# Kernel optimization log

Measured on AMD Instinct MI355X. Metric: run time of the kernel, lower is better.

Reference implementation:

```python
import jax, jax.numpy as jnp
import numpy as np

NUM_HEADS = 16
HEAD_DIM = 64
LN_EPS = 1e-5


def setup_inputs() -> dict:
    key = jax.random.key(0)
    k1, k2, k3, k4 = jax.random.split(key, 4)
    B, N, D = 4, 2048, NUM_HEADS * HEAD_DIM
    q = jax.random.normal(k1, (B, N, D), dtype=jnp.float32)
    k = jax.random.normal(k2, (B, N, D), dtype=jnp.float32)
    v = jax.random.normal(k3, (B, N, D), dtype=jnp.float32)
    W_out = jax.random.normal(k4, (D, D), dtype=jnp.float32) * (1.0 / np.sqrt(D))
    g = jnp.ones((D,), dtype=jnp.float32)
    return {"q": q, "k": k, "v": v, "W_out": W_out, "g": g}


def _split_heads(x):
    b, n, _ = x.shape
    return x.reshape(b, n, NUM_HEADS, HEAD_DIM).transpose(0, 2, 1, 3)  # b h n d


def reference(q, k, v, W_out, g):
    scale = HEAD_DIM ** -0.5
    qh = _split_heads(q) * scale          # [b,h,n,d]
    kh = _split_heads(k)                  # [b,h,m,d]
    vh = _split_heads(v)                  # [b,h,m,d]
    sim = jnp.einsum('bhnd,bhmd->bhnm', qh, kh)
    attn = jax.nn.softmax(sim.astype(jnp.float32), axis=-1)
    out = jnp.einsum('bhnm,bhmd->bhnd', attn, vh)
    b, h, n, d = out.shape
    out = out.transpose(0, 2, 1, 3).reshape(b, n, h * d)  # b n (h d)
    out = out @ W_out.T                   # Linear, no bias
    # LayerNorm (bias=False), biased variance
    mean = jnp.mean(out, axis=-1, keepdims=True)
    var = jnp.var(out, axis=-1, keepdims=True)
    return (out - mean) * jax.lax.rsqrt(var + LN_EPS) * g
```

## Files before the change

### kernel.cpp

```cpp
#include <hip/hip_runtime.h>
#include <hip/hip_bf16.h>


#define Bv 4
#define Nv 2048
#define Hv 16
#define DHv 64
#define Dv 1024
#define NT (Nv / 64)

#define KCONV_BLOCKS 4096
#define WCONV_BLOCKS 512
#define VT_BLOCKS 2048

#define L2E 1.44269504088896340736f

typedef __attribute__((ext_vector_type(8))) short short8;
typedef __attribute__((ext_vector_type(4))) float floatx4;

__device__ inline unsigned pack_bf2(float a, float b) {
    unsigned ua = __builtin_bit_cast(unsigned, a) + 0x8000u;
    unsigned ub = __builtin_bit_cast(unsigned, b) + 0x8000u;
    return __builtin_amdgcn_perm(ub, ua, 0x07060302u);
}

__device__ inline unsigned bf2u_rte(float a, float b) {
    unsigned short ua = __builtin_bit_cast(unsigned short, __float2bfloat16(a));
    unsigned short ub = __builtin_bit_cast(unsigned short, __float2bfloat16(b));
    return (unsigned)ua | ((unsigned)ub << 16);
}

__device__ inline void plswap16(unsigned &a, unsigned &b) {
    auto r = __builtin_amdgcn_permlane16_swap(a, b, false, false);
    a = r[0]; b = r[1];
}
__device__ inline void plswap32(unsigned &a, unsigned &b) {
    auto r = __builtin_amdgcn_permlane32_swap(a, b, false, false);
    a = r[0]; b = r[1];
}

__device__ inline float redq_max(float x) {
    unsigned a = __builtin_bit_cast(unsigned, x), b = a;
    plswap16(a, b);
    float m = fmaxf(__builtin_bit_cast(float, a), __builtin_bit_cast(float, b));
    unsigned c = __builtin_bit_cast(unsigned, m), d = c;
    plswap32(c, d);
    return fmaxf(__builtin_bit_cast(float, c), __builtin_bit_cast(float, d));
}
__device__ inline float redq_sum(float x) {
    unsigned a = __builtin_bit_cast(unsigned, x), b = a;
    plswap16(a, b);
    float m = __builtin_bit_cast(float, a) + __builtin_bit_cast(float, b);
    unsigned c = __builtin_bit_cast(unsigned, m), d = c;
    plswap32(c, d);
    return __builtin_bit_cast(float, c) + __builtin_bit_cast(float, d);
}

__global__ __launch_bounds__(256)
void prep_all(const float* __restrict__ K, __hip_bfloat16* __restrict__ Kb,
              const float* __restrict__ W, __hip_bfloat16* __restrict__ Wb,
              const float* __restrict__ v, __hip_bfloat16* __restrict__ vt) {
    __shared__ short T[64][72];
    int bid = blockIdx.x;
    if (bid < KCONV_BLOCKS + WCONV_BLOCKS) {
        const float* src;
        __hip_bfloat16* dst;
        if (bid < KCONV_BLOCKS) { src = K; dst = Kb; }
        else { src = W; dst = Wb; bid -= KCONV_BLOCKS; }
        int base = (bid * 256 + threadIdx.x) * 8;
        float4 f0 = *(const float4*)(src + base);
        float4 f1 = *(const float4*)(src + base + 4);
        uint4 u;
        u.x = pack_bf2(f0.x, f0.y);
        u.y = pack_bf2(f0.z, f0.w);
        u.z = pack_bf2(f1.x, f1.y);
        u.w = pack_bf2(f1.z, f1.w);
        *(uint4*)(dst + base) = u;
        return;
    }
    bid -= KCONV_BLOCKS + WCONV_BLOCKS;
    const int b = bid >> 9;
    const int rem = bid & 511;
    const int h = rem >> 5;
    const int n0 = (rem & 31) * 64;
    const int t = threadIdx.x;
    const int ir = t >> 4;
    const int d4 = (t & 15) * 4;
#pragma unroll
    for (int pass = 0; pass < 4; ++pass) {
        int n = pass * 16 + ir;
        float4 f = *(const float4*)(v + ((size_t)b * Nv + n0 + n) * Dv + h * DHv + d4);
        T[d4 + 0][n] = (short)(pack_bf2(f.x, f.x) & 0xffffu);
        T[d4 + 1][n] = (short)(pack_bf2(f.y, f.y) & 0xffffu);
        T[d4 + 2][n] = (short)(pack_bf2(f.z, f.z) & 0xffffu);
        T[d4 + 3][n] = (short)(pack_bf2(f.w, f.w) & 0xffffu);
    }
    __syncthreads();
    const int d = t >> 2, kg = (t & 3) * 16;
    unsigned u[8];
#pragma unroll
    for (int i = 0; i < 8; ++i)
        u[i] = (unsigned)(unsigned short)T[d][kg + 2 * i] |
               ((unsigned)(unsigned short)T[d][kg + 2 * i + 1] << 16);
    __hip_bfloat16* op = vt + ((size_t)(b * Hv + h) * DHv + d) * Nv + n0 + kg;
    *(uint4*)op = *(uint4*)&u[0];
    *(uint4*)(op + 8) = *(uint4*)&u[4];
}

__global__ __launch_bounds__(256)
void attn_mfma_pre(const float* __restrict__ q,
                   const __hip_bfloat16* __restrict__ Kb,
                   const __hip_bfloat16* __restrict__ Vtb,
                   __hip_bfloat16* __restrict__ out) {
    __shared__ __align__(16) short Kt[2][64 * 64];
    __shared__ __align__(16) short Vt[2][64 * 64];

    const int t = threadIdx.x;
    const int wave = t >> 6, lane = t & 63;
    const int quad = lane >> 4, lr = lane & 15;
    const int b = blockIdx.z;
    const int lid2 = blockIdx.y * 16 + blockIdx.x;
    const int xcd = lid2 & 7, jj = lid2 >> 3;
    const int h = xcd * 2 + (jj >> 4);
    const int q0 = (jj & 15) * 128;
    const size_t qbh = ((size_t)b * Nv) * Dv + h * DHv;
    const __hip_bfloat16* kb = Kb + (size_t)b * Nv * Dv + h * DHv;
    const __hip_bfloat16* vtb = Vtb + (size_t)(b * Hv + h) * DHv * Nv;

    const int srow = lane >> 3;
    const int sg = lane & 7;
    auto stage = [&](int buf, int k0) {
#pragma unroll
        for (int c = 0; c < 2; ++c) {
            int blk = wave * 2 + c;
            int r = blk * 8 + srow;
            int g = sg ^ (r & 7);
            __builtin_amdgcn_global_load_lds(
                (const __attribute__((address_space(1))) unsigned*)(const void*)
                    (kb + (size_t)(k0 + r) * Dv + g * 8),
                (__attribute__((address_space(3))) unsigned*)(void*)&Kt[buf][blk * 512],
                16, 0, 0);
            __builtin_amdgcn_global_load_lds(
                (const __attribute__((address_space(1))) unsigned*)(const void*)
                    (vtb + (size_t)r * Nv + k0 + g * 8),
                (__attribute__((address_space(3))) unsigned*)(void*)&Vt[buf][blk * 512],
                16, 0, 0);
        }
    };

    stage(0, 0);

    short8 qfrag[2][2];
#pragma unroll
    for (int qs = 0; qs < 2; ++qs)
#pragma unroll
        for (int kh = 0; kh < 2; ++kh) {
            int row = q0 + wave * 32 + qs * 16 + lr;
            const float* qp = q + qbh + (size_t)row * Dv + kh * 32 + quad * 8;
            float4 f0 = *(const float4*)qp;
            float4 f1 = *(const float4*)(qp + 4);
            int4 qi;
            qi.x = (int)pack_bf2(f0.x * 0.125f, f0.y * 0.125f);
            qi.y = (int)pack_bf2(f0.z * 0.125f, f0.w * 0.125f);
            qi.z = (int)pack_bf2(f1.x * 0.125f, f1.y * 0.125f);
            qi.w = (int)pack_bf2(f1.z * 0.125f, f1.w * 0.125f);
            qfrag[qs][kh] = __builtin_bit_cast(short8, qi);
        }

    floatx4 o_acc[2][4] = {};
    float mrow[2] = {-INFINITY, -INFINITY};
    float lrow[2] = {0.f, 0.f};

    for (int it = 0; it < NT; ++it) {
        const int cur = it & 1;
        __syncthreads();
        if (it + 1 < NT) stage(1 - cur, (it + 1) * 64);

        floatx4 s_acc[2][4] = {};
#pragma unroll
        for (int tt = 0; tt < 4; ++tt) {
            int row = tt * 16 + lr;
            short8 kf0 = *(const short8*)&Kt[cur][row * 64 + ((quad ^ (lr & 7)) << 3)];
            short8 kf1 = *(const short8*)&Kt[cur][row * 64 + (((4 + quad) ^ (lr & 7)) << 3)];
#pragma unroll
            for (int qs = 0; qs < 2; ++qs) {
                s_acc[qs][tt] = __builtin_amdgcn_mfma_f32_16x16x32_bf16(kf0, qfrag[qs][0], s_acc[qs][tt], 0, 0, 0);
                s_acc[qs][tt] = __builtin_amdgcn_mfma_f32_16x16x32_bf16(kf1, qfrag[qs][1], s_acc[qs][tt], 0, 0, 0);
            }
        }

        unsigned p2[2][8];
#pragma unroll
        for (int qs = 0; qs < 2; ++qs) {
            float t4[4];
#pragma unroll
            for (int tt = 0; tt < 4; ++tt)
                t4[tt] = fmaxf(fmaxf(s_acc[qs][tt][0], s_acc[qs][tt][1]),
                               fmaxf(s_acc[qs][tt][2], s_acc[qs][tt][3]));
            float tmax = fmaxf(fmaxf(t4[0], t4[1]), fmaxf(t4[2], t4[3]));
            tmax = redq_max(tmax);
            if (!__all(tmax <= mrow[qs] + 8.0f)) {
                float mnew = fmaxf(mrow[qs], tmax);
                float alpha = __expf(mrow[qs] - mnew);
                mrow[qs] = mnew;
                lrow[qs] *= alpha;
#pragma unroll
                for (int td = 0; td < 4; ++td)
#pragma unroll
                    for (int r2 = 0; r2 < 4; ++r2) o_acc[qs][td][r2] *= alpha;
            }
            float mc = mrow[qs] * L2E;
            float psum = 0.f;
#pragma unroll
            for (int tt = 0; tt < 4; ++tt)
#pragma unroll
                for (int r2 = 0; r2 < 4; ++r2) {
                    float p = __builtin_amdgcn_exp2f(__builtin_fmaf(s_acc[qs][tt][r2], L2E, -mc));
                    s_acc[qs][tt][r2] = p;
                    psum += p;
                }
            psum = redq_sum(psum);
            lrow[qs] += psum;
#pragma unroll
            for (int tt = 0; tt < 4; ++tt) {
                p2[qs][tt * 2 + 0] = pack_bf2(s_acc[qs][tt][0], s_acc[qs][tt][1]);
                p2[qs][tt * 2 + 1] = pack_bf2(s_acc[qs][tt][2], s_acc[qs][tt][3]);
            }
        }

#pragma unroll
        for (int kh = 0; kh < 2; ++kh) {
            short8 af[2];
#pragma unroll
            for (int qs = 0; qs < 2; ++qs) {
                int tlo = 4 * kh, thi = 4 * kh + 2;
                unsigned a0 = p2[qs][tlo + 0], b0 = p2[qs][thi + 0];
                unsigned a1 = p2[qs][tlo + 1], b1 = p2[qs][thi + 1];
                plswap32(a0, b0);
                plswap16(a0, b0);
                plswap32(a1, b1);
                plswap16(a1, b1);
                int4 afi;
                afi.x = (int)a0;
                afi.y = (int)a1;
                afi.z = (int)b0;
                afi.w = (int)b1;
                af[qs] = __builtin_bit_cast(short8, afi);
            }
#pragma unroll
            for (int td = 0; td < 4; ++td) {
                int d = td * 16 + lr;
                short8 vf = *(const short8*)&Vt[cur][d * 64 + (((kh * 4 + quad) ^ (lr & 7)) << 3)];
                o_acc[0][td] = __builtin_amdgcn_mfma_f32_16x16x32_bf16(vf, af[0], o_acc[0][td], 0, 0, 0);
                o_acc[1][td] = __builtin_amdgcn_mfma_f32_16x16x32_bf16(vf, af[1], o_acc[1][td], 0, 0, 0);
            }
        }
    }

#pragma unroll
    for (int qs = 0; qs < 2; ++qs) {
        float linv = 1.f / lrow[qs];
        int qrow = q0 + wave * 32 + qs * 16 + lr;
        __hip_bfloat16* op = out + ((size_t)(b * Nv + qrow)) * Dv + h * DHv + quad * 4;
#pragma unroll
        for (int td = 0; td < 4; ++td) {
            uint2 w;
            w.x = bf2u_rte(o_acc[qs][td][0] * linv, o_acc[qs][td][1] * linv);
            w.y = bf2u_rte(o_acc[qs][td][2] * linv, o_acc[qs][td][3] * linv);
            *(uint2*)(op + td * 16) = w;
        }
    }
}

__global__ __launch_bounds__(256)
void proj_kernel(const __hip_bfloat16* __restrict__ A,
                 const __hip_bfloat16* __restrict__ Wb,
                 float* __restrict__ C) {
    __shared__ __align__(16) short As[2][128 * 64];
    __shared__ __align__(16) short Ws[2][128 * 64];

    const int t = threadIdx.x;
    const int wave = t >> 6, lane = t & 63;
    const int quad = lane >> 4, lr = lane & 15;
    const int wm = wave >> 1, wn = wave & 1;
    const int bx = blockIdx.x;
    const int xcd = bx & 7, j = bx >> 3;
    const int bm = (xcd * 8 + (j >> 3)) * 128;
    const int bn = (j & 7) * 128;

    floatx4 acc[4][4] = {};

    auto stage = [&](int buf, int k0) {
#pragma unroll
        for (int c = 0; c < 4; ++c) {
            const int blk = c * 4 + wave;
            const int r = blk * 8 + (lane >> 3);
            const int g = (lane & 7) ^ (r & 7);
            const __hip_bfloat16* ga = A + (size_t)(bm + r) * Dv + k0 + g * 8;
            const __hip_bfloat16* gw = Wb + (size_t)(bn + r) * Dv + k0 + g * 8;
            __builtin_amdgcn_global_load_lds(
                (const __attribute__((address_space(1))) unsigned int*)(const void*)ga,
                (__attribute__((address_space(3))) unsigned int*)(void*)&As[buf][blk * 512],
                16, 0, 0);
            __builtin_amdgcn_global_load_lds(
                (const __attribute__((address_space(1))) unsigned int*)(const void*)gw,
                (__attribute__((address_space(3))) unsigned int*)(void*)&Ws[buf][blk * 512],
                16, 0, 0);
        }
    };

    stage(0, 0);

    for (int it = 0; it < Dv / 64; ++it) {
        const int cur = it & 1;
        __syncthreads();
        if (it + 1 < Dv / 64) stage(1 - cur, (it + 1) * 64);

#pragma unroll
        for (int ks = 0; ks < 2; ++ks) {
            short8 af[4];
#pragma unroll
            for (int mb = 0; mb < 4; ++mb) {
                int row = wm * 64 + mb * 16 + lr;
                af[mb] = *(const short8*)&As[cur][row * 64 + (((ks * 4 + quad) ^ (lr & 7)) << 3)];
            }
#pragma unroll
            for (int nb = 0; nb < 4; ++nb) {
                int row = wn * 64 + nb * 16 + lr;
                short8 bf = *(const short8*)&Ws[cur][row * 64 + (((ks * 4 + quad) ^ (lr & 7)) << 3)];
#pragma unroll
                for (int mb = 0; mb < 4; ++mb)
                    acc[mb][nb] = __builtin_amdgcn_mfma_f32_16x16x32_bf16(af[mb], bf, acc[mb][nb], 0, 0, 0);
            }
        }
    }

#pragma unroll
    for (int mb = 0; mb < 4; ++mb)
#pragma unroll
        for (int nb = 0; nb < 4; ++nb) {
            int row = bm + wm * 64 + mb * 16 + quad * 4;
            int col = bn + wn * 64 + nb * 16 + lr;
#pragma unroll
            for (int r = 0; r < 4; ++r)
                C[(size_t)(row + r) * Dv + col] = acc[mb][nb][r];
        }
}

__global__ __launch_bounds__(256)
void ln_kernel(float* __restrict__ C,
               const float* __restrict__ g) {
    const int row = blockIdx.x;
    const int t = threadIdx.x;
    const int wave = t >> 6, lane = t & 63;

    float* rp = C + (size_t)row * Dv;
    float4 x = *(const float4*)(rp + t * 4);

    float s = x.x + x.y + x.z + x.w;
    float sq = x.x * x.x + x.y * x.y + x.z * x.z + x.w * x.w;
#pragma unroll
    for (int off = 32; off >= 1; off >>= 1) {
        s += __shfl_xor(s, off);
        sq += __shfl_xor(sq, off);
    }
    __shared__ float ss[4], ssq[4];
    if (lane == 0) { ss[wave] = s; ssq[wave] = sq; }
    __syncthreads();
    s = ss[0] + ss[1] + ss[2] + ss[3];
    sq = ssq[0] + ssq[1] + ssq[2] + ssq[3];

    const float rn = 1.f / (float)Dv;
    float mean = s * rn;
    float var = sq * rn - mean * mean;
    float inv = rsqrtf(var + 1e-5f);

    float4 gv = *(const float4*)(g + t * 4);

    float4 o;
    o.x = (x.x - mean) * inv * gv.x;
    o.y = (x.y - mean) * inv * gv.y;
    o.z = (x.z - mean) * inv * gv.z;
    o.w = (x.w - mean) * inv * gv.w;
    *(float4*)(rp + t * 4) = o;
}

extern "C" void kernel_launch(void* const* d_in, const int* in_sizes, int n_in,
                              void* d_out, int out_size, void* d_ws, size_t ws_size,
                              hipStream_t stream) {
    const float* q = (const float*)d_in[0];
    const float* k = (const float*)d_in[1];
    const float* v = (const float*)d_in[2];
    const float* W = (const float*)d_in[3];
    const float* g = (const float*)d_in[4];
    float* out = (float*)d_out;

    const size_t attnB = (size_t)Bv * Nv * Dv * 2;
    const size_t wbB = (size_t)Dv * Dv * 2;
    const size_t kbB = (size_t)Bv * Nv * Dv * 2;

    __hip_bfloat16* attn = (__hip_bfloat16*)d_ws;
    __hip_bfloat16* Wb = (__hip_bfloat16*)((char*)d_ws + attnB);
    __hip_bfloat16* Kb = (__hip_bfloat16*)((char*)d_ws + attnB + wbB);
    __hip_bfloat16* Vtb = (__hip_bfloat16*)((char*)d_ws + attnB + wbB + kbB);

    prep_all<<<KCONV_BLOCKS + WCONV_BLOCKS + VT_BLOCKS, 256, 0, stream>>>(k, Kb, W, Wb, v, Vtb);
    attn_mfma_pre<<<dim3(16, 16, Bv), 256, 0, stream>>>(q, Kb, Vtb, attn);
    proj_kernel<<<512, 256, 0, stream>>>(attn, Wb, out);
    ln_kernel<<<Bv * Nv, 256, 0, stream>>>(out, g);
}
```

Before: 295.1 us.

## Use packed FMA and max3 in softmax, unroll main loops by two

Rewrites the online-softmax inner step to use inline-asm v_pk_fma_f32 for the exp2 argument and a max3 chain for the row max. It also fuses the exp, sum and bf16 pack into one loop. Adds unroll-by-2 on the attention and projection K loops and pads the transpose LDS tile from 72 to 76 columns. The aim is to cut VALU instruction count in the softmax critical path and loop overhead, at the cost of possible register pressure and of the asm blocking compiler scheduling.

```diff
diff --git a/kernel.cpp b/kernel.cpp
--- a/kernel.cpp
+++ b/kernel.cpp
@@ -17,6 +17,10 @@
 
 typedef __attribute__((ext_vector_type(8))) short short8;
 typedef __attribute__((ext_vector_type(4))) float floatx4;
+typedef __attribute__((ext_vector_type(2))) float float2v;
+
+#define LOPAIR(v) __builtin_shufflevector(v, v, 0, 1)
+#define HIPAIR(v) __builtin_shufflevector(v, v, 2, 3)
 
 __device__ inline unsigned pack_bf2(float a, float b) {
     unsigned ua = __builtin_bit_cast(unsigned, a) + 0x8000u;
@@ -28,6 +32,16 @@
     unsigned short ua = __builtin_bit_cast(unsigned short, __float2bfloat16(a));
     unsigned short ub = __builtin_bit_cast(unsigned short, __float2bfloat16(b));
     return (unsigned)ua | ((unsigned)ub << 16);
+}
+
+__device__ inline float2v pk_fma(float2v a, float2v b, float2v c) {
+    float2v d;
+    asm("v_pk_fma_f32 %0, %1, %2, %3" : "=v"(d) : "v"(a), "v"(b), "v"(c));
+    return d;
+}
+
+__device__ inline float max3f(float a, float b, float c) {
+    return fmaxf(fmaxf(a, b), c);
 }
 
 __device__ inline void plswap16(unsigned &a, unsigned &b) {
@@ -60,7 +74,7 @@
 void prep_all(const float* __restrict__ K, __hip_bfloat16* __restrict__ Kb,
               const float* __restrict__ W, __hip_bfloat16* __restrict__ Wb,
               const float* __restrict__ v, __hip_bfloat16* __restrict__ vt) {
-    __shared__ short T[64][72];
+    __shared__ short T[64][76];
     int bid = blockIdx.x;
     if (bid < KCONV_BLOCKS + WCONV_BLOCKS) {
         const float* src;
@@ -170,7 +184,9 @@
     floatx4 o_acc[2][4] = {};
     float mrow[2] = {-INFINITY, -INFINITY};
     float lrow[2] = {0.f, 0.f};
-
+    const float2v l2e2 = {L2E, L2E};
+
+#pragma unroll 2
     for (int it = 0; it < NT; ++it) {
         const int cur = it & 1;
         __syncthreads();
@@ -192,13 +208,13 @@
         unsigned p2[2][8];
 #pragma unroll
         for (int qs = 0; qs < 2; ++qs) {
-            float t4[4];
-#pragma unroll
-            for (int tt = 0; tt < 4; ++tt)
-                t4[tt] = fmaxf(fmaxf(s_acc[qs][tt][0], s_acc[qs][tt][1]),
-                               fmaxf(s_acc[qs][tt][2], s_acc[qs][tt][3]));
-            float tmax = fmaxf(fmaxf(t4[0], t4[1]), fmaxf(t4[2], t4[3]));
-            tmax = redq_max(tmax);
+            float m0 = max3f(s_acc[qs][0][0], s_acc[qs][0][1], s_acc[qs][0][2]);
+            float m1 = max3f(s_acc[qs][0][3], s_acc[qs][1][0], s_acc[qs][1][1]);
+            float m2 = max3f(s_acc[qs][1][2], s_acc[qs][1][3], s_acc[qs][2][0]);
+            float m3 = max3f(s_acc[qs][2][1], s_acc[qs][2][2], s_acc[qs][2][3]);
+            float m4 = max3f(s_acc[qs][3][0], s_acc[qs][3][1], s_acc[qs][3][2]);
+            float m5 = max3f(m0, m1, s_acc[qs][3][3]);
+            float tmax = redq_max(max3f(m5, max3f(m2, m3, m4), -INFINITY));
             if (!__all(tmax <= mrow[qs] + 8.0f)) {
                 float mnew = fmaxf(mrow[qs], tmax);
                 float alpha = __expf(mrow[qs] - mnew);
@@ -209,23 +225,22 @@
 #pragma unroll
                     for (int r2 = 0; r2 < 4; ++r2) o_acc[qs][td][r2] *= alpha;
             }
-            float mc = mrow[qs] * L2E;
+            float negmc = -(mrow[qs] * L2E);
+            float2v mcn2 = {negmc, negmc};
             float psum = 0.f;
 #pragma unroll
-            for (int tt = 0; tt < 4; ++tt)
-#pragma unroll
-                for (int r2 = 0; r2 < 4; ++r2) {
-                    float p = __builtin_amdgcn_exp2f(__builtin_fmaf(s_acc[qs][tt][r2], L2E, -mc));
-                    s_acc[qs][tt][r2] = p;
-                    psum += p;
-                }
-            psum = redq_sum(psum);
-            lrow[qs] += psum;
-#pragma unroll
             for (int tt = 0; tt < 4; ++tt) {
-                p2[qs][tt * 2 + 0] = pack_bf2(s_acc[qs][tt][0], s_acc[qs][tt][1]);
-                p2[qs][tt * 2 + 1] = pack_bf2(s_acc[qs][tt][2], s_acc[qs][tt][3]);
-            }
+                float2v e0 = pk_fma(LOPAIR(s_acc[qs][tt]), l2e2, mcn2);
+                float2v e1 = pk_fma(HIPAIR(s_acc[qs][tt]), l2e2, mcn2);
+                float p0 = __builtin_amdgcn_exp2f(e0.x);
+                float p1 = __builtin_amdgcn_exp2f(e0.y);
+                float p2v_ = __builtin_amdgcn_exp2f(e1.x);
+                float p3 = __builtin_amdgcn_exp2f(e1.y);
+                psum += (p0 + p1) + (p2v_ + p3);
+                p2[qs][tt * 2 + 0] = pack_bf2(p0, p1);
+                p2[qs][tt * 2 + 1] = pack_bf2(p2v_, p3);
+            }
+            lrow[qs] += redq_sum(psum);
         }
 
 #pragma unroll
@@ -311,6 +326,7 @@
 
     stage(0, 0);
 
+#pragma unroll 2
     for (int it = 0; it < Dv / 64; ++it) {
         const int cur = it & 1;
         __syncthreads();
```

After: 289.7 us. No clear change (-1.8%).

## Halve attention query tile per block to raise occupancy, add setprio and unrolling

Applied to the files above, without the earlier changes.

The attention kernel now gives each wave a single 16-row query slice instead of two. Blocks cover 64 query rows and the grid doubles, with launch bounds asking for 8 blocks per CU. This cuts accumulator register pressure and adds parallelism, but every K/V tile is reloaded through LDS twice as often per query. It also wraps the MFMA sections in s_setprio, restructures the max reduction with max3, unrolls the main loops by 2 in both the attention and projection kernels, and pads the transpose LDS tile in prep.

```diff
diff --git a/kernel.cpp b/kernel.cpp
--- a/kernel.cpp
+++ b/kernel.cpp
@@ -28,6 +28,10 @@
     unsigned short ua = __builtin_bit_cast(unsigned short, __float2bfloat16(a));
     unsigned short ub = __builtin_bit_cast(unsigned short, __float2bfloat16(b));
     return (unsigned)ua | ((unsigned)ub << 16);
+}
+
+__device__ inline float max3f(float a, float b, float c) {
+    return fmaxf(fmaxf(a, b), c);
 }
 
 __device__ inline void plswap16(unsigned &a, unsigned &b) {
@@ -60,7 +64,7 @@
 void prep_all(const float* __restrict__ K, __hip_bfloat16* __restrict__ Kb,
               const float* __restrict__ W, __hip_bfloat16* __restrict__ Wb,
               const float* __restrict__ v, __hip_bfloat16* __restrict__ vt) {
-    __shared__ short T[64][72];
+    __shared__ short T[64][76];
     int bid = blockIdx.x;
     if (bid < KCONV_BLOCKS + WCONV_BLOCKS) {
         const float* src;
@@ -107,7 +111,7 @@
     *(uint4*)(op + 8) = *(uint4*)&u[4];
 }
 
-__global__ __launch_bounds__(256)
+__global__ __launch_bounds__(256, 8)
 void attn_mfma_pre(const float* __restrict__ q,
                    const __hip_bfloat16* __restrict__ Kb,
                    const __hip_bfloat16* __restrict__ Vtb,
@@ -119,10 +123,10 @@
     const int wave = t >> 6, lane = t & 63;
     const int quad = lane >> 4, lr = lane & 15;
     const int b = blockIdx.z;
-    const int lid2 = blockIdx.y * 16 + blockIdx.x;
+    const int lid2 = blockIdx.y * 32 + blockIdx.x;
     const int xcd = lid2 & 7, jj = lid2 >> 3;
-    const int h = xcd * 2 + (jj >> 4);
-    const int q0 = (jj & 15) * 128;
+    const int h = xcd * 2 + (jj >> 5);
+    const int q0 = (jj & 31) * 64;
     const size_t qbh = ((size_t)b * Nv) * Dv + h * DHv;
     const __hip_bfloat16* kb = Kb + (size_t)b * Nv * Dv + h * DHv;
     const __hip_bfloat16* vtb = Vtb + (size_t)(b * Hv + h) * DHv * Nv;
@@ -150,123 +154,110 @@
 
     stage(0, 0);
 
-    short8 qfrag[2][2];
-#pragma unroll
-    for (int qs = 0; qs < 2; ++qs)
-#pragma unroll
-        for (int kh = 0; kh < 2; ++kh) {
-            int row = q0 + wave * 32 + qs * 16 + lr;
-            const float* qp = q + qbh + (size_t)row * Dv + kh * 32 + quad * 8;
-            float4 f0 = *(const float4*)qp;
-            float4 f1 = *(const float4*)(qp + 4);
-            int4 qi;
-            qi.x = (int)pack_bf2(f0.x * 0.125f, f0.y * 0.125f);
-            qi.y = (int)pack_bf2(f0.z * 0.125f, f0.w * 0.125f);
-            qi.z = (int)pack_bf2(f1.x * 0.125f, f1.y * 0.125f);
-            qi.w = (int)pack_bf2(f1.z * 0.125f, f1.w * 0.125f);
-            qfrag[qs][kh] = __builtin_bit_cast(short8, qi);
-        }
-
-    floatx4 o_acc[2][4] = {};
-    float mrow[2] = {-INFINITY, -INFINITY};
-    float lrow[2] = {0.f, 0.f};
-
+    short8 qfrag[2];
+#pragma unroll
+    for (int kh = 0; kh < 2; ++kh) {
+        int row = q0 + wave * 16 + lr;
+        const float* qp = q + qbh + (size_t)row * Dv + kh * 32 + quad * 8;
+        float4 f0 = *(const float4*)qp;
+        float4 f1 = *(const float4*)(qp + 4);
+        int4 qi;
+        qi.x = (int)pack_bf2(f0.x * 0.125f, f0.y * 0.125f);
+        qi.y = (int)pack_bf2(f0.z * 0.125f, f0.w * 0.125f);
+        qi.z = (int)pack_bf2(f1.x * 0.125f, f1.y * 0.125f);
+        qi.w = (int)pack_bf2(f1.z * 0.125f, f1.w * 0.125f);
+        qfrag[kh] = __builtin_bit_cast(short8, qi);
+    }
+
+    floatx4 o_acc[4] = {};
+    float mrow = -INFINITY;
+    float lrow = 0.f;
+
+#pragma unroll 2
     for (int it = 0; it < NT; ++it) {
         const int cur = it & 1;
         __syncthreads();
         if (it + 1 < NT) stage(1 - cur, (it + 1) * 64);
 
-        floatx4 s_acc[2][4] = {};
+        floatx4 s_acc[4] = {};
+        __builtin_amdgcn_s_setprio(1);
 #pragma unroll
         for (int tt = 0; tt < 4; ++tt) {
             int row = tt * 16 + lr;
             short8 kf0 = *(const short8*)&Kt[cur][row * 64 + ((quad ^ (lr & 7)) << 3)];
             short8 kf1 = *(const short8*)&Kt[cur][row * 64 + (((4 + quad) ^ (lr & 7)) << 3)];
-#pragma unroll
-            for (int qs = 0; qs < 2; ++qs) {
-                s_acc[qs][tt] = __builtin_amdgcn_mfma_f32_16x16x32_bf16(kf0, qfrag[qs][0], s_acc[qs][tt], 0, 0, 0);
-                s_acc[qs][tt] = __builtin_amdgcn_mfma_f32_16x16x32_bf16(kf1, qfrag[qs][1], s_acc[qs][tt], 0, 0, 0);
-            }
-        }
-
-        unsigned p2[2][8];
-#pragma unroll
-        for (int qs = 0; qs < 2; ++qs) {
-            float t4[4];
-#pragma unroll
-            for (int tt = 0; tt < 4; ++tt)
-                t4[tt] = fmaxf(fmaxf(s_acc[qs][tt][0], s_acc[qs][tt][1]),
-                               fmaxf(s_acc[qs][tt][2], s_acc[qs][tt][3]));
-            float tmax = fmaxf(fmaxf(t4[0], t4[1]), fmaxf(t4[2], t4[3]));
-            tmax = redq_max(tmax);
-            if (!__all(tmax <= mrow[qs] + 8.0f)) {
-                float mnew = fmaxf(mrow[qs], tmax);
-                float alpha = __expf(mrow[qs] - mnew);
-                mrow[qs] = mnew;
-                lrow[qs] *= alpha;
-#pragma unroll
-                for (int td = 0; td < 4; ++td)
-#pragma unroll
-                    for (int r2 = 0; r2 < 4; ++r2) o_acc[qs][td][r2] *= alpha;
-            }
-            float mc = mrow[qs] * L2E;
-            float psum = 0.f;
-#pragma unroll
-            for (int tt = 0; tt < 4; ++tt)
-#pragma unroll
-                for (int r2 = 0; r2 < 4; ++r2) {
-                    float p = __builtin_amdgcn_exp2f(__builtin_fmaf(s_acc[qs][tt][r2], L2E, -mc));
-                    s_acc[qs][tt][r2] = p;
-                    psum += p;
-                }
-            psum = redq_sum(psum);
-            lrow[qs] += psum;
-#pragma unroll
-            for (int tt = 0; tt < 4; ++tt) {
-                p2[qs][tt * 2 + 0] = pack_bf2(s_acc[qs][tt][0], s_acc[qs][tt][1]);
-                p2[qs][tt * 2 + 1] = pack_bf2(s_acc[qs][tt][2], s_acc[qs][tt][3]);
-            }
-        }
+            s_acc[tt] = __builtin_amdgcn_mfma_f32_16x16x32_bf16(kf0, qfrag[0], s_acc[tt], 0, 0, 0);
+            s_acc[tt] = __builtin_amdgcn_mfma_f32_16x16x32_bf16(kf1, qfrag[1], s_acc[tt], 0, 0, 0);
+        }
+        __builtin_amdgcn_s_setprio(0);
+
+        float m0 = max3f(s_acc[0][0], s_acc[0][1], s_acc[0][2]);
+        float m1 = max3f(s_acc[0][3], s_acc[1][0], s_acc[1][1]);
+        float m2 = max3f(s_acc[1][2], s_acc[1][3], s_acc[2][0]);
+        float m3 = max3f(s_acc[2][1], s_acc[2][2], s_acc[2][3]);
+        float m4 = max3f(s_acc[3][0], s_acc[3][1], s_acc[3][2]);
+        float m5 = max3f(m0, m1, s_acc[3][3]);
+        float tmax = redq_max(max3f(m5, max3f(m2, m3, m4), -INFINITY));
+        if (!__all(tmax <= mrow + 8.0f)) {
+            float mnew = fmaxf(mrow, tmax);
+            float alpha = __expf(mrow - mnew);
+            mrow = mnew;
+            lrow *= alpha;
+#pragma unroll
+            for (int td = 0; td < 4; ++td)
+#pragma unroll
+                for (int r2 = 0; r2 < 4; ++r2) o_acc[td][r2] *= alpha;
+        }
+        float negmc = -(mrow * L2E);
+        unsigned p2[8];
+        float psum = 0.f;
+#pragma unroll
+        for (int tt = 0; tt < 4; ++tt) {
+            float p0 = __builtin_amdgcn_exp2f(__builtin_fmaf(s_acc[tt][0], L2E, negmc));
+            float p1 = __builtin_amdgcn_exp2f(__builtin_fmaf(s_acc[tt][1], L2E, negmc));
+            float pa = __builtin_amdgcn_exp2f(__builtin_fmaf(s_acc[tt][2], L2E, negmc));
+            float pb = __builtin_amdgcn_exp2f(__builtin_fmaf(s_acc[tt][3], L2E, negmc));
+            psum += (p0 + p1) + (pa + pb);
+            p2[tt * 2 + 0] = pack_bf2(p0, p1);
+            p2[tt * 2 + 1] = pack_bf2(pa, pb);
+        }
+        lrow += redq_sum(psum);
 
 #pragma unroll
         for (int kh = 0; kh < 2; ++kh) {
-            short8 af[2];
-#pragma unroll
-            for (int qs = 0; qs < 2; ++qs) {
-                int tlo = 4 * kh, thi = 4 * kh + 2;
-                unsigned a0 = p2[qs][tlo + 0], b0 = p2[qs][thi + 0];
-                unsigned a1 = p2[qs][tlo + 1], b1 = p2[qs][thi + 1];
-                plswap32(a0, b0);
-                plswap16(a0, b0);
-                plswap32(a1, b1);
-                plswap16(a1, b1);
-                int4 afi;
-                afi.x = (int)a0;
-                afi.y = (int)a1;
-                afi.z = (int)b0;
-                afi.w = (int)b1;
-                af[qs] = __builtin_bit_cast(short8, afi);
-            }
+            int tlo = 4 * kh, thi = 4 * kh + 2;
+            unsigned a0 = p2[tlo + 0], b0 = p2[thi + 0];
+            unsigned a1 = p2[tlo + 1], b1 = p2[thi + 1];
+            plswap32(a0, b0);
+            plswap16(a0, b0);
+            plswap32(a1, b1);
+            plswap16(a1, b1);
+            int4 afi;
+            afi.x = (int)a0;
+            afi.y = (int)a1;
+            afi.z = (int)b0;
+            afi.w = (int)b1;
+            short8 af = __builtin_bit_cast(short8, afi);
+            __builtin_amdgcn_s_setprio(1);
 #pragma unroll
             for (int td = 0; td < 4; ++td) {
                 int d = td * 16 + lr;
                 short8 vf = *(const short8*)&Vt[cur][d * 64 + (((kh * 4 + quad) ^ (lr & 7)) << 3)];
-                o_acc[0][td] = __builtin_amdgcn_mfma_f32_16x16x32_bf16(vf, af[0], o_acc[0][td], 0, 0, 0);
-                o_acc[1][td] = __builtin_amdgcn_mfma_f32_16x16x32_bf16(vf, af[1], o_acc[1][td], 0, 0, 0);
+                o_acc[td] = __builtin_amdgcn_mfma_f32_16x16x32_bf16(vf, af, o_acc[td], 0, 0, 0);
             }
-        }
-    }
-
-#pragma unroll
-    for (int qs = 0; qs < 2; ++qs) {
-        float linv = 1.f / lrow[qs];
-        int qrow = q0 + wave * 32 + qs * 16 + lr;
+            __builtin_amdgcn_s_setprio(0);
+        }
+    }
+
+    {
+        float linv = 1.f / lrow;
+        int qrow = q0 + wave * 16 + lr;
         __hip_bfloat16* op = out + ((size_t)(b * Nv + qrow)) * Dv + h * DHv + quad * 4;
 #pragma unroll
         for (int td = 0; td < 4; ++td) {
             uint2 w;
-            w.x = bf2u_rte(o_acc[qs][td][0] * linv, o_acc[qs][td][1] * linv);
-            w.y = bf2u_rte(o_acc[qs][td][2] * linv, o_acc[qs][td][3] * linv);
+            w.x = bf2u_rte(o_acc[td][0] * linv, o_acc[td][1] * linv);
+            w.y = bf2u_rte(o_acc[td][2] * linv, o_acc[td][3] * linv);
             *(uint2*)(op + td * 16) = w;
         }
     }
@@ -311,6 +302,7 @@
 
     stage(0, 0);
 
+#pragma unroll 2
     for (int it = 0; it < Dv / 64; ++it) {
         const int cur = it & 1;
         __syncthreads();
@@ -405,7 +397,7 @@
     __hip_bfloat16* Vtb = (__hip_bfloat16*)((char*)d_ws + attnB + wbB + kbB);
 
     prep_all<<<KCONV_BLOCKS + WCONV_BLOCKS + VT_BLOCKS, 256, 0, stream>>>(k, Kb, W, Wb, v, Vtb);
-    attn_mfma_pre<<<dim3(16, 16, Bv), 256, 0, stream>>>(q, Kb, Vtb, attn);
+    attn_mfma_pre<<<dim3(32, 16, Bv), 256, 0, stream>>>(q, Kb, Vtb, attn);
     proj_kernel<<<512, 256, 0, stream>>>(attn, Wb, out);
     ln_kernel<<<Bv * Nv, 256, 0, stream>>>(out, g);
 }
```

After: 288.2 us. 2.3% less time.
